# Kernel optimization log

Hardware: AMD Instinct MI355X
Metric: run time of the kernel (lower is better)

The kernel has to match this reference:

```python
import jax, jax.numpy as jnp
import numpy as np

B, D, G, H = 65536, 512, 16, 128


def setup_inputs() -> dict:
    key = jax.random.key(0)
    ks = jax.random.split(key, 8)
    s = 1.0 / np.sqrt(D)
    sh = 1.0 / np.sqrt(H)
    return {
        "z": jax.random.normal(ks[0], (B, D), dtype=jnp.float32),
        "Wc": jax.random.uniform(ks[1], (D, G), jnp.float32, -s, s),
        "bc": jax.random.uniform(ks[2], (G,), jnp.float32, -s, s),
        "W1": jax.random.uniform(ks[3], (G, D, H), jnp.float32, -s, s),
        "b1": jax.random.uniform(ks[4], (G, H), jnp.float32, -s, s),
        "W2": jax.random.uniform(ks[5], (G, H), jnp.float32, -sh, sh),
        "b2": jax.random.uniform(ks[6], (G,), jnp.float32, -sh, sh),
    }


def reference(z, Wc, bc, W1, b1, W2, b2):
    # classifier head + softmax
    logits = z @ Wc + bc                                  # [B, G]
    p_g = jax.nn.softmax(logits, axis=1)                  # [B, G]
    # G experts fused as one batched GEMM: fc1 -> GELU -> fc2 (dropout = identity at eval)
    h = jax.nn.gelu(jnp.einsum('bd,gdh->bgh', z, W1) + b1, approximate=False)  # [B, G, H]
    y_all = jnp.einsum('bgh,gh->bg', h, W2) + b2          # [B, G]
    return logits, p_g, y_all
```

## Files before the change

kernel.cpp:

```cpp
#include <hip/hip_runtime.h>
#include <cstdint>
#include <cstddef>

typedef __bf16 bf16x8 __attribute__((ext_vector_type(8)));
typedef float f32x4 __attribute__((ext_vector_type(4)));
typedef unsigned short ushortx8 __attribute__((ext_vector_type(8)));

__device__ __forceinline__ unsigned short f2bf(float f) {
  union { float f; unsigned int u; } v; v.f = f;
  return (unsigned short)((v.u + 0x8000u) >> 16);
}

__device__ __forceinline__ float gelu_f(float x) {
  float t = 0.7978845608f * x * (1.0f + 0.044715f * x * x);
  float e = __expf(-2.0f * fabsf(t));
  float th = (1.0f - e) / (1.0f + e);
  th = (t >= 0.0f) ? th : -th;
  return 0.5f * x * (1.0f + th);
}

#define GLOAD16(gsrc, ldst)                                                  \
  __builtin_amdgcn_global_load_lds(                                          \
      (const __attribute__((address_space(1))) unsigned int*)(gsrc),         \
      (__attribute__((address_space(3))) unsigned int*)(uintptr_t)(          \
          (char*)(ldst)),                                                    \
      16, 0, 0)

#define SWZ_FRAG(base, R, C8)                                                \
  (*(const bf16x8*)((base) + (((R) >> 5) * 4096) +                           \
                    ((((R)&31) * 8 + ((C8) ^ ((R)&7))) * 16)))

__global__ __launch_bounds__(256) void k_convert(
    const float* __restrict__ z, const float* __restrict__ W1,
    const float* __restrict__ Wc, unsigned short* __restrict__ zb,
    unsigned short* __restrict__ w1t, unsigned short* __restrict__ wct) {
  int bid = blockIdx.x;
  int tid = threadIdx.x;
  if (bid < 16384) {
    size_t i = ((size_t)bid * 256 + tid) * 8;
    const float4* p = (const float4*)(z + i);
    float4 a = p[0], b = p[1];
    ushortx8 r;
    r[0] = f2bf(a.x); r[1] = f2bf(a.y); r[2] = f2bf(a.z); r[3] = f2bf(a.w);
    r[4] = f2bf(b.x); r[5] = f2bf(b.y); r[6] = f2bf(b.z); r[7] = f2bf(b.w);
    *(ushortx8*)(zb + i) = r;
  } else if (bid < 16384 + 4096) {
    int i = (bid - 16384) * 256 + tid;
    int d = i & 511;
    int h = (i >> 9) & 127;
    int gg = i >> 16;
    w1t[i] = f2bf(W1[(gg << 16) + d * 128 + h]);
  } else {
    int i = (bid - 20480) * 256 + tid;
    int gg = i >> 9;
    int d = i & 511;
    wct[i] = f2bf(Wc[d * 16 + gg]);
  }
}

__global__ __launch_bounds__(256, 2) void k_main(
    const unsigned short* __restrict__ zb,
    const unsigned short* __restrict__ w1t,
    const unsigned short* __restrict__ wct,
    const float* __restrict__ bc, const float* __restrict__ b1,
    const float* __restrict__ w2, const float* __restrict__ b2,
    float* __restrict__ out) {
  __shared__ alignas(16) char lds[16384 + 16384 + 1024];
  const int tid = threadIdx.x;
  const int g = blockIdx.x % 17;
  const int m = blockIdx.x / 17;
  const int mbase = m * 128;
  const int wv = tid >> 6;
  const int ln = tid & 63;
  const int l15 = ln & 15;
  const int l4 = ln >> 4;

  const int c8s = (((tid & 7) ^ ((tid >> 3) & 7))) * 8;
  const unsigned short* ag = zb + (size_t)(mbase + (tid >> 3)) * 512 + c8s;

  if (g < 16) {
    const unsigned short* bg = w1t + g * 65536 + (tid >> 3) * 512 + c8s;
    const int rh = (wv >> 1) * 64;
    const int ch = (wv & 1) * 64;
    f32x4 acc[4][4] = {};
    for (int kt = 0; kt < 8; ++kt) {
      const int ko = kt * 64;
#pragma unroll
      for (int it = 0; it < 4; ++it) {
        GLOAD16(ag + (size_t)it * 32 * 512 + ko, lds + it * 4096 + tid * 16);
        GLOAD16(bg + it * 32 * 512 + ko,
                lds + 16384 + it * 4096 + tid * 16);
      }
      __syncthreads();
      bf16x8 af[4][2], bfv[4][2];
#pragma unroll
      for (int rt = 0; rt < 4; ++rt)
#pragma unroll
        for (int ks = 0; ks < 2; ++ks)
          af[rt][ks] = SWZ_FRAG(lds, rh + rt * 16 + l15, ks * 4 + l4);
#pragma unroll
      for (int ct = 0; ct < 4; ++ct)
#pragma unroll
        for (int ks = 0; ks < 2; ++ks)
          bfv[ct][ks] =
              SWZ_FRAG(lds + 16384, ch + ct * 16 + l15, ks * 4 + l4);
#pragma unroll
      for (int rt = 0; rt < 4; ++rt)
#pragma unroll
        for (int ct = 0; ct < 4; ++ct)
#pragma unroll
          for (int ks = 0; ks < 2; ++ks)
            acc[rt][ct] = __builtin_amdgcn_mfma_f32_16x16x32_bf16(
                af[rt][ks], bfv[ct][ks], acc[rt][ct], 0, 0, 0);
      __syncthreads();
    }
    float b1v[4], w2v[4];
#pragma unroll
    for (int ct = 0; ct < 4; ++ct) {
      int n = ch + ct * 16 + l15;
      b1v[ct] = b1[g * 128 + n];
      w2v[ct] = w2[g * 128 + n];
    }
    float* ylds = (float*)(lds + 32768);
#pragma unroll
    for (int rt = 0; rt < 4; ++rt) {
#pragma unroll
      for (int i = 0; i < 4; ++i) {
        float s = 0.0f;
#pragma unroll
        for (int ct = 0; ct < 4; ++ct) {
          float x = acc[rt][ct][i] + b1v[ct];
          s += gelu_f(x) * w2v[ct];
        }
#pragma unroll
        for (int off = 1; off < 16; off <<= 1)
          s += __shfl_xor(s, off, 16);
        if (l15 == 0) ylds[(wv & 1) * 128 + rh + rt * 16 + l4 * 4 + i] = s;
      }
    }
    __syncthreads();
    if (tid < 128) {
      float y = ylds[tid] + ylds[128 + tid] + b2[g];
      out[(size_t)2097152 + (size_t)(mbase + tid) * 16 + g] = y;
    }
  } else {
#pragma unroll
    for (int it = 0; it < 4; ++it)
      GLOAD16(wct + it * 2048 + tid * 8, lds + 16384 + it * 4096 + tid * 16);
    f32x4 acc2[2] = {};
    for (int kt = 0; kt < 8; ++kt) {
      const int ko = kt * 64;
#pragma unroll
      for (int it = 0; it < 4; ++it)
        GLOAD16(ag + (size_t)it * 32 * 512 + ko, lds + it * 4096 + tid * 16);
      __syncthreads();
      bf16x8 bfr[2];
#pragma unroll
      for (int ks = 0; ks < 2; ++ks)
        bfr[ks] = *(const bf16x8*)(lds + 16384 + l15 * 1024 +
                                   (ko + ks * 32 + l4 * 8) * 2);
#pragma unroll
      for (int rt = 0; rt < 2; ++rt)
#pragma unroll
        for (int ks = 0; ks < 2; ++ks) {
          bf16x8 af = SWZ_FRAG(lds, wv * 32 + rt * 16 + l15, ks * 4 + l4);
          acc2[rt] = __builtin_amdgcn_mfma_f32_16x16x32_bf16(af, bfr[ks],
                                                             acc2[rt], 0, 0, 0);
        }
      __syncthreads();
    }
    float bcv = bc[l15];
#pragma unroll
    for (int rt = 0; rt < 2; ++rt) {
#pragma unroll
      for (int i = 0; i < 4; ++i) {
        int row = wv * 32 + rt * 16 + l4 * 4 + i;
        float lg = acc2[rt][i] + bcv;
        float mx = lg;
#pragma unroll
        for (int off = 1; off < 16; off <<= 1)
          mx = fmaxf(mx, __shfl_xor(mx, off, 16));
        float e = __expf(lg - mx);
        float sm = e;
#pragma unroll
        for (int off = 1; off < 16; off <<= 1)
          sm += __shfl_xor(sm, off, 16);
        size_t ro = (size_t)(mbase + row) * 16 + l15;
        out[ro] = lg;
        out[1048576 + ro] = e / sm;
      }
    }
  }
}

extern "C" void kernel_launch(void* const* d_in, const int* in_sizes, int n_in,
                              void* d_out, int out_size, void* d_ws,
                              size_t ws_size, hipStream_t stream) {
  const float* z = (const float*)d_in[0];
  const float* Wc = (const float*)d_in[1];
  const float* bc = (const float*)d_in[2];
  const float* W1 = (const float*)d_in[3];
  const float* b1 = (const float*)d_in[4];
  const float* W2 = (const float*)d_in[5];
  const float* b2 = (const float*)d_in[6];
  float* out = (float*)d_out;

  unsigned short* zb = (unsigned short*)d_ws;
  unsigned short* w1t = zb + (size_t)65536 * 512;
  unsigned short* wct = w1t + (size_t)16 * 128 * 512;

  k_convert<<<16384 + 4096 + 32, 256, 0, stream>>>(z, W1, Wc, zb, w1t, wct);
  k_main<<<512 * 17, 256, 0, stream>>>(zb, w1t, wct, bc, b1, W2, b2, out);
}
```

Measured before the change: 418.9 us.

## Process two experts per block and tile the W1 transpose through LDS

The main GEMM kernel now handles two experts per block (128 rows x 256 hidden columns), with each wave covering one full expert's 128 columns. This cuts how often the z tile is reloaded and removes the cross-wave LDS reduction of the fc2 partial sums. Block order is also changed so that one expert pair sweeps across all row tiles. The weight conversion kernel now transposes W1 through a padded shared-memory tile for coalesced access, and Wc is converted by a single block. In exchange, each thread holds twice as many accumulators (32 f32x4), which raises register pressure and may lower occupancy under the launch bound of 2.

```diff
diff --git a/kernel.cpp b/kernel.cpp
--- a/kernel.cpp
+++ b/kernel.cpp
@@ -44,17 +44,31 @@
     r[0] = f2bf(a.x); r[1] = f2bf(a.y); r[2] = f2bf(a.z); r[3] = f2bf(a.w);
     r[4] = f2bf(b.x); r[5] = f2bf(b.y); r[6] = f2bf(b.z); r[7] = f2bf(b.w);
     *(ushortx8*)(zb + i) = r;
-  } else if (bid < 16384 + 4096) {
-    int i = (bid - 16384) * 256 + tid;
-    int d = i & 511;
-    int h = (i >> 9) & 127;
-    int gg = i >> 16;
-    w1t[i] = f2bf(W1[(gg << 16) + d * 128 + h]);
+  } else if (bid < 16384 + 1024) {
+    __shared__ float tile[32][33];
+    int b = bid - 16384;
+    int gg = b >> 6;
+    int t = b & 63;
+    int d0 = (t >> 2) * 32;
+    int h0 = (t & 3) * 32;
+    int tx = tid & 31, ty = tid >> 5;
+#pragma unroll
+    for (int r = 0; r < 4; ++r) {
+      int d = d0 + r * 8 + ty;
+      tile[r * 8 + ty][tx] = W1[(gg << 16) + d * 128 + h0 + tx];
+    }
+    __syncthreads();
+#pragma unroll
+    for (int r = 0; r < 4; ++r) {
+      int h = h0 + r * 8 + ty;
+      w1t[(gg << 16) + h * 512 + d0 + tx] = f2bf(tile[tx][r * 8 + ty]);
+    }
   } else {
-    int i = (bid - 20480) * 256 + tid;
-    int gg = i >> 9;
-    int d = i & 511;
-    wct[i] = f2bf(Wc[d * 16 + gg]);
+#pragma unroll
+    for (int j = 0; j < 32; ++j) {
+      int i = j * 256 + tid;
+      wct[(i & 15) * 512 + (i >> 4)] = f2bf(Wc[i]);
+    }
   }
 }
 
@@ -65,10 +79,10 @@
     const float* __restrict__ bc, const float* __restrict__ b1,
     const float* __restrict__ w2, const float* __restrict__ b2,
     float* __restrict__ out) {
-  __shared__ alignas(16) char lds[16384 + 16384 + 1024];
+  __shared__ alignas(16) char lds[16384 + 32768];
   const int tid = threadIdx.x;
-  const int g = blockIdx.x % 17;
-  const int m = blockIdx.x / 17;
+  const int p = blockIdx.x >> 9;
+  const int m = blockIdx.x & 511;
   const int mbase = m * 128;
   const int wv = tid >> 6;
   const int ln = tid & 63;
@@ -77,76 +91,74 @@
 
   const int c8s = (((tid & 7) ^ ((tid >> 3) & 7))) * 8;
   const unsigned short* ag = zb + (size_t)(mbase + (tid >> 3)) * 512 + c8s;
-
-  if (g < 16) {
-    const unsigned short* bg = w1t + g * 65536 + (tid >> 3) * 512 + c8s;
-    const int rh = (wv >> 1) * 64;
-    const int ch = (wv & 1) * 64;
-    f32x4 acc[4][4] = {};
+  char* ldsB = lds + 16384;
+
+  if (p < 8) {
+    const unsigned short* bg =
+        w1t + p * 131072 + (tid >> 3) * 512 + c8s;
+    const int wr = wv >> 1;
+    const int wc = wv & 1;
+    const int e = p * 2 + wc;
+    const int rowb = wr * 64;
+    const int colb = wc * 128;
+    f32x4 acc[4][8] = {};
     for (int kt = 0; kt < 8; ++kt) {
       const int ko = kt * 64;
 #pragma unroll
-      for (int it = 0; it < 4; ++it) {
+      for (int it = 0; it < 4; ++it)
         GLOAD16(ag + (size_t)it * 32 * 512 + ko, lds + it * 4096 + tid * 16);
-        GLOAD16(bg + it * 32 * 512 + ko,
-                lds + 16384 + it * 4096 + tid * 16);
+#pragma unroll
+      for (int it = 0; it < 8; ++it)
+        GLOAD16(bg + it * 32 * 512 + ko, ldsB + it * 4096 + tid * 16);
+      __syncthreads();
+#pragma unroll
+      for (int ks = 0; ks < 2; ++ks) {
+        bf16x8 af[4];
+#pragma unroll
+        for (int rt = 0; rt < 4; ++rt)
+          af[rt] = SWZ_FRAG(lds, rowb + rt * 16 + l15, ks * 4 + l4);
+#pragma unroll
+        for (int ct = 0; ct < 8; ++ct) {
+          bf16x8 bf = SWZ_FRAG(ldsB, colb + ct * 16 + l15, ks * 4 + l4);
+#pragma unroll
+          for (int rt = 0; rt < 4; ++rt)
+            acc[rt][ct] = __builtin_amdgcn_mfma_f32_16x16x32_bf16(
+                af[rt], bf, acc[rt][ct], 0, 0, 0);
+        }
       }
       __syncthreads();
-      bf16x8 af[4][2], bfv[4][2];
-#pragma unroll
-      for (int rt = 0; rt < 4; ++rt)
-#pragma unroll
-        for (int ks = 0; ks < 2; ++ks)
-          af[rt][ks] = SWZ_FRAG(lds, rh + rt * 16 + l15, ks * 4 + l4);
-#pragma unroll
-      for (int ct = 0; ct < 4; ++ct)
-#pragma unroll
-        for (int ks = 0; ks < 2; ++ks)
-          bfv[ct][ks] =
-              SWZ_FRAG(lds + 16384, ch + ct * 16 + l15, ks * 4 + l4);
-#pragma unroll
-      for (int rt = 0; rt < 4; ++rt)
-#pragma unroll
-        for (int ct = 0; ct < 4; ++ct)
-#pragma unroll
-          for (int ks = 0; ks < 2; ++ks)
-            acc[rt][ct] = __builtin_amdgcn_mfma_f32_16x16x32_bf16(
-                af[rt][ks], bfv[ct][ks], acc[rt][ct], 0, 0, 0);
-      __syncthreads();
-    }
-    float b1v[4], w2v[4];
-#pragma unroll
-    for (int ct = 0; ct < 4; ++ct) {
-      int n = ch + ct * 16 + l15;
-      b1v[ct] = b1[g * 128 + n];
-      w2v[ct] = w2[g * 128 + n];
-    }
-    float* ylds = (float*)(lds + 32768);
+    }
+    float b1v[8], w2v[8];
+#pragma unroll
+    for (int ct = 0; ct < 8; ++ct) {
+      int n = ct * 16 + l15;
+      b1v[ct] = b1[e * 128 + n];
+      w2v[ct] = w2[e * 128 + n];
+    }
+    float b2v = b2[e];
 #pragma unroll
     for (int rt = 0; rt < 4; ++rt) {
 #pragma unroll
       for (int i = 0; i < 4; ++i) {
         float s = 0.0f;
 #pragma unroll
-        for (int ct = 0; ct < 4; ++ct) {
+        for (int ct = 0; ct < 8; ++ct) {
           float x = acc[rt][ct][i] + b1v[ct];
           s += gelu_f(x) * w2v[ct];
         }
 #pragma unroll
         for (int off = 1; off < 16; off <<= 1)
           s += __shfl_xor(s, off, 16);
-        if (l15 == 0) ylds[(wv & 1) * 128 + rh + rt * 16 + l4 * 4 + i] = s;
+        if (l15 == 0) {
+          int row = rowb + rt * 16 + l4 * 4 + i;
+          out[(size_t)2097152 + (size_t)(mbase + row) * 16 + e] = s + b2v;
+        }
       }
     }
-    __syncthreads();
-    if (tid < 128) {
-      float y = ylds[tid] + ylds[128 + tid] + b2[g];
-      out[(size_t)2097152 + (size_t)(mbase + tid) * 16 + g] = y;
-    }
   } else {
 #pragma unroll
     for (int it = 0; it < 4; ++it)
-      GLOAD16(wct + it * 2048 + tid * 8, lds + 16384 + it * 4096 + tid * 16);
+      GLOAD16(wct + it * 2048 + tid * 8, ldsB + it * 4096 + tid * 16);
     f32x4 acc2[2] = {};
     for (int kt = 0; kt < 8; ++kt) {
       const int ko = kt * 64;
@@ -157,7 +169,7 @@
       bf16x8 bfr[2];
 #pragma unroll
       for (int ks = 0; ks < 2; ++ks)
-        bfr[ks] = *(const bf16x8*)(lds + 16384 + l15 * 1024 +
+        bfr[ks] = *(const bf16x8*)(ldsB + l15 * 1024 +
                                    (ko + ks * 32 + l4 * 8) * 2);
 #pragma unroll
       for (int rt = 0; rt < 2; ++rt)
@@ -180,14 +192,14 @@
 #pragma unroll
         for (int off = 1; off < 16; off <<= 1)
           mx = fmaxf(mx, __shfl_xor(mx, off, 16));
-        float e = __expf(lg - mx);
-        float sm = e;
+        float ex = __expf(lg - mx);
+        float sm = ex;
 #pragma unroll
         for (int off = 1; off < 16; off <<= 1)
           sm += __shfl_xor(sm, off, 16);
         size_t ro = (size_t)(mbase + row) * 16 + l15;
         out[ro] = lg;
-        out[1048576 + ro] = e / sm;
+        out[1048576 + ro] = ex / sm;
       }
     }
   }
@@ -209,6 +221,6 @@
   unsigned short* w1t = zb + (size_t)65536 * 512;
   unsigned short* wct = w1t + (size_t)16 * 128 * 512;
 
-  k_convert<<<16384 + 4096 + 32, 256, 0, stream>>>(z, W1, Wc, zb, w1t, wct);
-  k_main<<<512 * 17, 256, 0, stream>>>(zb, w1t, wct, bc, b1, W2, b2, out);
-}
+  k_convert<<<16384 + 1024 + 1, 256, 0, stream>>>(z, W1, Wc, zb, w1t, wct);
+  k_main<<<9 * 512, 256, 0, stream>>>(zb, w1t, wct, bc, b1, W2, b2, out);
+}
```

Measured after the change: 429.6 us. 2.6% more time.
